# Kernel tuning notes

Measured on AMD Instinct MI355X. Metric: run time of the kernel, lower is better.

Reference implementation:

```python
import jax, jax.numpy as jnp
import numpy as np
import math

EMB = 64
NEG_INF = -1e30

def _layernorm(x, g, b, eps=1e-5):
    mu = jnp.mean(x, axis=-1, keepdims=True)
    var = jnp.mean((x - mu) ** 2, axis=-1, keepdims=True)
    return (x - mu) * jax.lax.rsqrt(var + eps) * g + b

def setup_inputs() -> dict:
    key = jax.random.key(0)
    ks = jax.random.split(key, 8)
    b, t, n, d = 16, 12, 307, EMB
    s = 1.0 / math.sqrt(d)
    inp = {
        'x': jax.random.normal(ks[0], (b, t, n, d), dtype=jnp.float32),
        'stg': jax.random.uniform(ks[1], (b, n, t, n), dtype=jnp.float32),
        'topk': 3,
        'q_w': jax.random.normal(ks[2], (d, d), dtype=jnp.float32) * s,
        'q_b': jnp.zeros((d,), jnp.float32),
        'k_w': jax.random.normal(ks[3], (d, d), dtype=jnp.float32) * s,
        'k_b': jnp.zeros((d,), jnp.float32),
        'ln_g': jnp.ones((d,), jnp.float32),
        'ln_b': jnp.zeros((d,), jnp.float32),
        'ffn_ln_g': jnp.ones((d,), jnp.float32),
        'ffn_ln_b': jnp.zeros((d,), jnp.float32),
        'fc1_w': jax.random.normal(ks[4], (4 * d, d), dtype=jnp.float32) * s,
        'fc1_b': jnp.zeros((4 * d,), jnp.float32),
        'fc2_w': jax.random.normal(ks[5], (d, 4 * d), dtype=jnp.float32) * (0.5 * s),
        'fc2_b': jnp.zeros((d,), jnp.float32),
    }
    return inp

def reference(x, stg, topk, q_w, q_b, k_w, k_b, ln_g, ln_b, ffn_ln_g, ffn_ln_b, fc1_w, fc1_b, fc2_w, fc2_b):
    b, t, n, d = x.shape
    scale = 1.0 / math.sqrt(d)
    x_ = _layernorm(x, ln_g, ln_b)           # [b,t,n,d]
    y_ = x_[:, -1]                            # [b,n,d] last timestep
    q = y_ @ q_w.T + q_b                      # [b,n,d]
    k = x_ @ k_w.T + k_b                      # [b,t,n,d]
    dg = jnp.einsum('bnd,btmd->bntm', q, k) * scale
    sag = jax.nn.sigmoid(dg) * stg * scale    # gated scores [b,n,t,n]
    sag = sag.reshape(b, n, t * n)
    if topk > 0:
        kk = topk * n if topk < 5 else topk   # mirrors torch's self.topk *= n
        top_values, _ = jax.lax.top_k(sag, kk)
        thr = top_values[..., -1:]
        sag = jnp.where(sag > thr, sag, NEG_INF)  # strict >, as in torch code
    sag = jax.nn.softmax(sag, axis=-1).reshape(b, n, t, n)  # dropout in eval mode = identity
    o = jnp.einsum('bntm,btmd->bnd', sag, x_)
    h = o + y_
    # FFN: pre-norm residual MLP (LayerNorm -> Linear(d,4d) -> ReLU -> Linear(4d,d) + residual)
    z = _layernorm(h, ffn_ln_g, ffn_ln_b)
    z = jax.nn.relu(z @ fc1_w.T + fc1_b) @ fc2_w.T + fc2_b
    return h + z
```

## Files before the change

### kernel.cpp

```cpp
#include <hip/hip_runtime.h>

typedef __bf16 bf16x8 __attribute__((ext_vector_type(8)));
typedef float  f32x4  __attribute__((ext_vector_type(4)));
typedef unsigned short u16x8 __attribute__((ext_vector_type(8)));

constexpr int BB    = 16;
constexpr int TT    = 12;
constexpr int NN    = 307;
constexpr int TN    = TT * NN;
constexpr int ROWSX = BB * TT * NN;
constexpr int ROWSH = BB * NN;
constexpr int SST1  = 3712;
constexpr int SSTR  = 3840;
constexpr int HPS   = ROWSH * 64;
constexpr int KQ    = 928;
constexpr float SCALE = 0.125f;

__device__ __forceinline__ float wred_sum(float v) {
#pragma unroll
    for (int m = 32; m > 0; m >>= 1) v += __shfl_xor(v, m, 64);
    return v;
}

__global__ void fold_k(const float* __restrict__ qw, const float* __restrict__ qb,
                       const float* __restrict__ kw, const float* __restrict__ kb,
                       float* __restrict__ M, float* __restrict__ b2,
                       float* __restrict__ vv, float* __restrict__ cc) {
    int e = blockIdx.x, d = threadIdx.x;
    float acc = 0.f;
    for (int dp = 0; dp < 64; ++dp) acc += qw[dp * 64 + e] * kw[dp * 64 + d];
    M[e * 64 + d] = acc;
    float vp = wred_sum(qw[d * 64 + e] * kb[d]);
    if (d == 0) vv[e] = vp;
    if (e == 0) {
        float b = 0.f;
        for (int dp = 0; dp < 64; ++dp) b += qb[dp] * kw[dp * 64 + d];
        b2[d] = b;
        float cp = wred_sum(qb[d] * kb[d]);
        if (d == 0) *cc = cp;
    }
}

__global__ void wconv_k(const float* __restrict__ fc1w, const float* __restrict__ fc2w,
                        __bf16* __restrict__ fc1b16, __bf16* __restrict__ fc2b16) {
    int i = blockIdx.x * 256 + threadIdx.x;
    if (i < 16384) fc1b16[i] = (__bf16)fc1w[i];
    else fc2b16[i - 16384] = (__bf16)fc2w[i - 16384];
}

__global__ __launch_bounds__(256) void ln_k(const float* __restrict__ x,
                                            const float* __restrict__ g,
                                            const float* __restrict__ b,
                                            __bf16* __restrict__ xnb,
                                            float* __restrict__ y32) {
    int w = threadIdx.x >> 6, l = threadIdx.x & 63;
    int r = blockIdx.x * 4 + w;
    if (r >= ROWSX) return;
    float val = x[r * 64 + l];
    float mu  = wred_sum(val) * (1.f / 64.f);
    float dv  = val - mu;
    float var = wred_sum(dv * dv) * (1.f / 64.f);
    float xv  = dv * rsqrtf(var + 1e-5f) * g[l] + b[l];
    xnb[(size_t)r * 64 + l] = (__bf16)xv;
    int t = (r / NN) % TT;
    if (t == TT - 1) {
        int bbv = r / (NN * TT), n = r % NN;
        y32[(bbv * NN + n) * 64 + l] = xv;
    }
}

__global__ __launch_bounds__(256) void t_k(const __bf16* __restrict__ xnb,
                                           __bf16* __restrict__ xnT) {
    __shared__ unsigned short tile[64][65];
    int bb = blockIdx.y, j0 = blockIdx.x * 64, t = threadIdx.x;
    const unsigned short* src = (const unsigned short*)xnb;
    unsigned short* dst = (unsigned short*)xnT;
#pragma unroll
    for (int i = 0; i < 16; ++i) {
        int f = t + 256 * i, jr = f >> 6, dc = f & 63;
        int j = j0 + jr;
        tile[jr][dc] = (j < TN) ? src[((size_t)bb * TN + j) * 64 + dc] : (unsigned short)0;
    }
    __syncthreads();
#pragma unroll
    for (int i = 0; i < 16; ++i) {
        int f = t + 256 * i, d = f >> 6, jj = f & 63;
        dst[((size_t)bb * 64 + d) * SSTR + j0 + jj] = tile[jj][d];
    }
}

__global__ __launch_bounds__(256) void qt_k(const float* __restrict__ y32,
                                            const float* __restrict__ M,
                                            const float* __restrict__ b2,
                                            const float* __restrict__ vv,
                                            const float* __restrict__ ccp,
                                            __bf16* __restrict__ qtb,
                                            float* __restrict__ cq) {
    int w = threadIdx.x >> 6, l = threadIdx.x & 63;
    int rr = blockIdx.x * 4 + w;
    if (rr >= ROWSH) return;
    float y = y32[rr * 64 + l];
    float acc = b2[l];
#pragma unroll
    for (int e = 0; e < 64; ++e) acc += __shfl(y, e, 64) * M[e * 64 + l];
    qtb[(size_t)rr * 64 + l] = (__bf16)acc;
    float cp = wred_sum(y * vv[l]);
    if (l == 0) cq[rr] = cp + *ccp;
}

__global__ __launch_bounds__(256) void score_k(const __bf16* __restrict__ qtb,
                                               const float* __restrict__ cq,
                                               const __bf16* __restrict__ xnb,
                                               const float* __restrict__ stg,
                                               __bf16* __restrict__ sag) {
    __shared__ unsigned short wb[64 * 136];
    int bb = blockIdx.z, n0 = blockIdx.y * 64, j0 = blockIdx.x * 128;
    int t = threadIdx.x;
    int w = t >> 6, lane = t & 63;
    int m16 = lane & 15, q4 = lane >> 4;

    const bf16x8* ap = (const bf16x8*)(qtb + ((size_t)bb * NN + n0 + w * 16 + m16) * 64);
    bf16x8 a0 = ap[q4], a1 = ap[q4 + 4];
    f32x4 acc[8];
#pragma unroll
    for (int jt = 0; jt < 8; ++jt) {
        const bf16x8* bp = (const bf16x8*)(xnb + ((size_t)bb * TN + j0 + jt * 16 + m16) * 64);
        bf16x8 b0 = bp[q4], b1 = bp[q4 + 4];
        f32x4 c = {0.f, 0.f, 0.f, 0.f};
        c = __builtin_amdgcn_mfma_f32_16x16x32_bf16(a0, b0, c, 0, 0, 0);
        c = __builtin_amdgcn_mfma_f32_16x16x32_bf16(a1, b1, c, 0, 0, 0);
        acc[jt] = c;
    }
    int nbase = n0 + w * 16 + q4 * 4;
    float cn[4];
#pragma unroll
    for (int r = 0; r < 4; ++r) {
        int n = nbase + r;
        cn[r] = (n < NN) ? cq[bb * NN + n] : 0.f;
    }

    const float* stgb = stg + (size_t)bb * NN * TN;
#pragma unroll
    for (int r = 0; r < 4; ++r) {
        int nloc = w * 16 + q4 * 4 + r;
        const float* srow = stgb + (size_t)min(nbase + r, NN - 1) * TN;
        u16x8 wvr;
#pragma unroll
        for (int jt = 0; jt < 8; ++jt) {
            int j = j0 + jt * 16 + m16;
            float sv = (j < TN) ? srow[j] : 0.f;
            float dg = (acc[jt][r] + cn[r]) * SCALE;
            float s  = 1.f / (1.f + __expf(-dg));
            float wv = (j < TN) ? s * sv * SCALE : 0.f;
            __bf16 wb16 = (__bf16)wv;
            wvr[jt] = *(unsigned short*)&wb16;
        }
#pragma unroll
        for (int jt = 0; jt < 8; ++jt)
            wb[nloc * 136 + jt * 16 + m16] = wvr[jt];
    }
    __syncthreads();

#pragma unroll
    for (int i = 0; i < 4; ++i) {
        int chunk = t + i * 256;
        int row = chunk >> 4, c8 = (chunk & 15) * 8;
        int n = n0 + row;
        if (n < NN) {
            u16x8 v = *(const u16x8*)&wb[row * 136 + c8];
            *(u16x8*)((unsigned short*)sag + (size_t)(bb * NN + n) * SST1 + j0 + c8) = v;
        }
    }
}

__global__ __launch_bounds__(256) void smax_k(__bf16* __restrict__ sagB,
                                              const int* __restrict__ topk_p,
                                              float* __restrict__ rsum) {
    int t = threadIdx.x;
    int wid = t >> 6, lane = t & 63;
    int row = blockIdx.x * 4 + wid;
    if (row >= ROWSH) return;

    int topkv = *topk_p;
    bool selAll = (topkv <= 0);
    int kk = 0;
    if (!selAll) {
        kk = (topkv < 5) ? topkv * NN : topkv;
        if (kk > TN) kk = TN;
    }

    u16x8* src = (u16x8*)((unsigned short*)sagB + (size_t)row * SST1);
    u16x8 va[8];
#pragma unroll
    for (int ci = 0; ci < 8; ++ci) {
        int c = lane + (ci << 6);
        u16x8 v = {0, 0, 0, 0, 0, 0, 0, 0};
        if (c < 464) v = src[c];
        va[ci] = v;
    }
    int vmb = 0;
#pragma unroll
    for (int ci = 0; ci < 8; ++ci)
#pragma unroll
        for (int e = 0; e < 8; ++e) vmb = max(vmb, (int)va[ci][e]);
#pragma unroll
    for (int m = 32; m > 0; m >>= 1) vmb = max(vmb, __shfl_xor(vmb, m, 64));
    float vmax = __uint_as_float(((unsigned)vmb) << 16);

    unsigned thrb = 0;
    if (!selAll) {
        unsigned lo = 0, hi = (unsigned)vmb;
        while (lo < hi) {
            unsigned mid = (lo + hi) >> 1;
            int cnt = 0;
#pragma unroll
            for (int ci = 0; ci < 8; ++ci)
#pragma unroll
                for (int e = 0; e < 8; ++e)
                    cnt += (int)__popcll(__ballot((unsigned)va[ci][e] > mid));
            if (cnt < kk) hi = mid; else lo = mid + 1;
        }
        thrb = lo;
    }

    float local = 0.f;
#pragma unroll
    for (int ci = 0; ci < 8; ++ci) {
        int c = lane + (ci << 6);
        int nvv = (c < 460) ? 8 : ((c == 460) ? 4 : 0);
#pragma unroll
        for (int e = 0; e < 8; ++e) {
            unsigned u = va[ci][e];
            bool sel = selAll ? (e < nvv) : (u > thrb);
            float ev = sel ? __expf(__uint_as_float(u << 16) - vmax) : 0.f;
            local += ev;
            __bf16 eb = (__bf16)ev;
            va[ci][e] = *(unsigned short*)&eb;
        }
    }
    local = wred_sum(local);
    bool uni = !(local > 0.f);
    if (lane == 0) rsum[row] = uni ? (float)TN : local;

    if (uni) {
        __bf16 one = (__bf16)1.f, zero = (__bf16)0.f;
#pragma unroll
        for (int ci = 0; ci < 8; ++ci) {
            int c = lane + (ci << 6);
            if (c < 464) {
                int nvv = (c < 460) ? 8 : ((c == 460) ? 4 : 0);
                bf16x8 o;
#pragma unroll
                for (int e = 0; e < 8; ++e) o[e] = (e < nvv) ? one : zero;
                *(bf16x8*)&src[c] = o;
            }
        }
    } else {
#pragma unroll
        for (int ci = 0; ci < 8; ++ci) {
            int c = lane + (ci << 6);
            if (c < 464) src[c] = va[ci];
        }
    }
}

__global__ __launch_bounds__(256) void pv_k(const __bf16* __restrict__ sagB,
                                            const __bf16* __restrict__ xnT,
                                            const float* __restrict__ y32,
                                            const float* __restrict__ rsum,
                                            float* __restrict__ hp) {
    int bb = blockIdx.z, kq = blockIdx.y, n0 = blockIdx.x * 16;
    int wid = threadIdx.x >> 6, lane = threadIdx.x & 63;
    int m16 = lane & 15, q4 = lane >> 4;

    int arow = min(n0 + m16, NN - 1);
    const __bf16* ab  = sagB + (size_t)(bb * NN + arow) * SST1 + kq * KQ + q4 * 8;
    const __bf16* bbp = xnT + ((size_t)bb * 64 + wid * 16 + m16) * SSTR + kq * KQ + q4 * 8;

    f32x4 acc0 = {0.f, 0.f, 0.f, 0.f}, acc1 = {0.f, 0.f, 0.f, 0.f};
#pragma unroll 4
    for (int ks = 0; ks < 29; ++ks) {
        bf16x8 a = *(const bf16x8*)(ab + ks * 32);
        bf16x8 b = *(const bf16x8*)(bbp + ks * 32);
        if (ks & 1) acc1 = __builtin_amdgcn_mfma_f32_16x16x32_bf16(a, b, acc1, 0, 0, 0);
        else        acc0 = __builtin_amdgcn_mfma_f32_16x16x32_bf16(a, b, acc0, 0, 0, 0);
    }
#pragma unroll
    for (int r = 0; r < 4; ++r) {
        int n = n0 + q4 * 4 + r;
        if (n < NN) {
            size_t o = (size_t)(bb * NN + n) * 64 + wid * 16 + m16;
            float inv = 1.f / rsum[bb * NN + n];
            float v = (acc0[r] + acc1[r]) * inv;
            if (kq == 0) v += y32[o];
            hp[(size_t)kq * HPS + o] = v;
        }
    }
}

__global__ __launch_bounds__(256) void ffn_k(const float* __restrict__ hp,
                                             const float* __restrict__ g,
                                             const float* __restrict__ bln,
                                             const __bf16* __restrict__ fc1b16,
                                             const float* __restrict__ fc1b,
                                             const __bf16* __restrict__ fc2b16,
                                             const float* __restrict__ fc2b,
                                             float* __restrict__ out) {
    __shared__ __bf16 zb[16 * 68];
    __shared__ __bf16 ab[16 * 264];
    int t = threadIdx.x, r0 = blockIdx.x * 16;
    int wid = t >> 6, lane = t & 63;
    int m16 = lane & 15, q4 = lane >> 4;

#pragma unroll
    for (int q = 0; q < 4; ++q) {
        int rl = wid * 4 + q;
        size_t i = (size_t)(r0 + rl) * 64 + lane;
        float val = hp[i] + hp[HPS + i] + hp[2 * HPS + i] + hp[3 * HPS + i];
        float mu  = wred_sum(val) * (1.f / 64.f);
        float dv  = val - mu;
        float var = wred_sum(dv * dv) * (1.f / 64.f);
        zb[rl * 68 + lane] = (__bf16)(dv * rsqrtf(var + 1e-5f) * g[lane] + bln[lane]);
    }
    __syncthreads();

    bf16x8 a0 = *(const bf16x8*)&zb[m16 * 68 + q4 * 8];
    bf16x8 a1 = *(const bf16x8*)&zb[m16 * 68 + 32 + q4 * 8];
#pragma unroll
    for (int jt2 = 0; jt2 < 4; ++jt2) {
        int j0t = (wid * 4 + jt2) * 16;
        const __bf16* bp = fc1b16 + (size_t)(j0t + m16) * 64 + q4 * 8;
        f32x4 c = {0.f, 0.f, 0.f, 0.f};
        c = __builtin_amdgcn_mfma_f32_16x16x32_bf16(a0, *(const bf16x8*)bp, c, 0, 0, 0);
        c = __builtin_amdgcn_mfma_f32_16x16x32_bf16(a1, *(const bf16x8*)(bp + 32), c, 0, 0, 0);
        int j = j0t + m16;
        float bias = fc1b[j];
#pragma unroll
        for (int r = 0; r < 4; ++r)
            ab[(q4 * 4 + r) * 264 + j] = (__bf16)fmaxf(c[r] + bias, 0.f);
    }
    __syncthreads();

    f32x4 c2a = {0.f, 0.f, 0.f, 0.f}, c2b = {0.f, 0.f, 0.f, 0.f};
    const __bf16* b2p = fc2b16 + (size_t)(wid * 16 + m16) * 256 + q4 * 8;
#pragma unroll
    for (int k8 = 0; k8 < 8; k8 += 2) {
        bf16x8 aa0 = *(const bf16x8*)&ab[m16 * 264 + k8 * 32 + q4 * 8];
        bf16x8 aa1 = *(const bf16x8*)&ab[m16 * 264 + (k8 + 1) * 32 + q4 * 8];
        c2a = __builtin_amdgcn_mfma_f32_16x16x32_bf16(aa0, *(const bf16x8*)(b2p + k8 * 32), c2a, 0, 0, 0);
        c2b = __builtin_amdgcn_mfma_f32_16x16x32_bf16(aa1, *(const bf16x8*)(b2p + (k8 + 1) * 32), c2b, 0, 0, 0);
    }
    int d = wid * 16 + m16;
    float bias2 = fc2b[d];
#pragma unroll
    for (int r = 0; r < 4; ++r) {
        size_t row = (size_t)(r0 + q4 * 4 + r);
        size_t o = row * 64 + d;
        float hsum = hp[o] + hp[HPS + o] + hp[2 * HPS + o] + hp[3 * HPS + o];
        out[o] = hsum + c2a[r] + c2b[r] + bias2;
    }
}

extern "C" void kernel_launch(void* const* d_in, const int* in_sizes, int n_in,
                              void* d_out, int out_size, void* d_ws, size_t ws_size,
                              hipStream_t stream) {
    const float* x    = (const float*)d_in[0];
    const float* stg  = (const float*)d_in[1];
    const int*   topk = (const int*)d_in[2];
    const float* qw   = (const float*)d_in[3];
    const float* qb   = (const float*)d_in[4];
    const float* kw   = (const float*)d_in[5];
    const float* kb   = (const float*)d_in[6];
    const float* lng  = (const float*)d_in[7];
    const float* lnb  = (const float*)d_in[8];
    const float* flng = (const float*)d_in[9];
    const float* flnb = (const float*)d_in[10];
    const float* fc1w = (const float*)d_in[11];
    const float* fc1b = (const float*)d_in[12];
    const float* fc2w = (const float*)d_in[13];
    const float* fc2b = (const float*)d_in[14];
    float* out = (float*)d_out;

    float* ws = (float*)d_ws;
    __bf16* xnb = (__bf16*)ws;
    float* p1   = ws + 1886208;
    __bf16* xnT = (__bf16*)p1;
    float* p2   = p1 + 1966080;
    __bf16* qtb = (__bf16*)p2;
    float* y32  = p2 + 157696;
    float* cq   = y32 + 314368;
    float* M    = cq + 4928;
    float* b2   = M + 4096;
    float* vv   = b2 + 64;
    float* cc   = vv + 64;
    __bf16* fc1b16 = (__bf16*)(cc + 16);
    __bf16* fc2b16 = (__bf16*)((float*)fc1b16 + 8192);
    __bf16* sag = (__bf16*)((float*)fc2b16 + 8192);
    float* hp   = (float*)sag + 9116672;
    float* rsum = hp + 4 * HPS;

    fold_k<<<64, 64, 0, stream>>>(qw, qb, kw, kb, M, b2, vv, cc);
    wconv_k<<<128, 256, 0, stream>>>(fc1w, fc2w, fc1b16, fc2b16);
    ln_k<<<(ROWSX + 3) / 4, 256, 0, stream>>>(x, lng, lnb, xnb, y32);
    t_k<<<dim3((TN + 63) / 64, BB), 256, 0, stream>>>(xnb, xnT);
    qt_k<<<(ROWSH + 3) / 4, 256, 0, stream>>>(y32, M, b2, vv, cc, qtb, cq);
    score_k<<<dim3((TN + 127) / 128, (NN + 63) / 64, BB), 256, 0, stream>>>(qtb, cq, xnb, stg, sag);
    smax_k<<<(ROWSH + 3) / 4, 256, 0, stream>>>(sag, topk, rsum);
    pv_k<<<dim3((NN + 15) / 16, 4, BB), 256, 0, stream>>>(sag, xnT, y32, rsum, hp);
    ffn_k<<<ROWSH / 16, 256, 0, stream>>>(hp, flng, flnb, fc1b16, fc1b, fc2b16, fc2b, out);
}
```

Before: 269.0 us.

## Fuse layernorm with transpose and swap MFMA operands for coalesced stg loads

Merges the layernorm kernel and the transpose kernel into one, so normalized rows go straight into the shared-memory tile and the transpose no longer has to re-read xnb from global memory. It also swaps the MFMA operand roles in score_k so that each lane's output elements lie along j. That lets stg be read with float4 loads and the bf16 results be written to LDS as 4-wide stores, with the row padding changed to 144. The cost is a smaller LN grid that does serial wave reductions per row.

Result: no change. 266.4 us (-1.0%).

```diff
diff --git a/kernel.cpp b/kernel.cpp
--- a/kernel.cpp
+++ b/kernel.cpp
@@ -3,6 +3,7 @@
 typedef __bf16 bf16x8 __attribute__((ext_vector_type(8)));
 typedef float  f32x4  __attribute__((ext_vector_type(4)));
 typedef unsigned short u16x8 __attribute__((ext_vector_type(8)));
+typedef unsigned short u16x4 __attribute__((ext_vector_type(4)));
 
 constexpr int BB    = 16;
 constexpr int TT    = 12;
@@ -48,38 +49,35 @@
     else fc2b16[i - 16384] = (__bf16)fc2w[i - 16384];
 }
 
-__global__ __launch_bounds__(256) void ln_k(const float* __restrict__ x,
-                                            const float* __restrict__ g,
-                                            const float* __restrict__ b,
-                                            __bf16* __restrict__ xnb,
-                                            float* __restrict__ y32) {
-    int w = threadIdx.x >> 6, l = threadIdx.x & 63;
-    int r = blockIdx.x * 4 + w;
-    if (r >= ROWSX) return;
-    float val = x[r * 64 + l];
-    float mu  = wred_sum(val) * (1.f / 64.f);
-    float dv  = val - mu;
-    float var = wred_sum(dv * dv) * (1.f / 64.f);
-    float xv  = dv * rsqrtf(var + 1e-5f) * g[l] + b[l];
-    xnb[(size_t)r * 64 + l] = (__bf16)xv;
-    int t = (r / NN) % TT;
-    if (t == TT - 1) {
-        int bbv = r / (NN * TT), n = r % NN;
-        y32[(bbv * NN + n) * 64 + l] = xv;
-    }
-}
-
-__global__ __launch_bounds__(256) void t_k(const __bf16* __restrict__ xnb,
-                                           __bf16* __restrict__ xnT) {
+__global__ __launch_bounds__(256) void lnt_k(const float* __restrict__ x,
+                                             const float* __restrict__ g,
+                                             const float* __restrict__ b,
+                                             __bf16* __restrict__ xnb,
+                                             __bf16* __restrict__ xnT,
+                                             float* __restrict__ y32) {
     __shared__ unsigned short tile[64][65];
     int bb = blockIdx.y, j0 = blockIdx.x * 64, t = threadIdx.x;
-    const unsigned short* src = (const unsigned short*)xnb;
+    int w = t >> 6, lane = t & 63;
+    float gg = g[lane], bbv = b[lane];
     unsigned short* dst = (unsigned short*)xnT;
-#pragma unroll
+#pragma unroll 4
     for (int i = 0; i < 16; ++i) {
-        int f = t + 256 * i, jr = f >> 6, dc = f & 63;
+        int jr = w * 16 + i;
         int j = j0 + jr;
-        tile[jr][dc] = (j < TN) ? src[((size_t)bb * TN + j) * 64 + dc] : (unsigned short)0;
+        bool valid = (j < TN);
+        float val = valid ? x[((size_t)bb * TN + j) * 64 + lane] : 0.f;
+        float mu  = wred_sum(val) * (1.f / 64.f);
+        float dv  = val - mu;
+        float var = wred_sum(dv * dv) * (1.f / 64.f);
+        float xv  = dv * rsqrtf(var + 1e-5f) * gg + bbv;
+        if (valid) {
+            __bf16 xb = (__bf16)xv;
+            xnb[((size_t)bb * TN + j) * 64 + lane] = xb;
+            tile[jr][lane] = *(unsigned short*)&xb;
+            if (j >= 11 * NN) y32[((size_t)bb * NN + (j - 11 * NN)) * 64 + lane] = xv;
+        } else {
+            tile[jr][lane] = 0;
+        }
     }
     __syncthreads();
 #pragma unroll
@@ -113,51 +111,57 @@
                                                const __bf16* __restrict__ xnb,
                                                const float* __restrict__ stg,
                                                __bf16* __restrict__ sag) {
-    __shared__ unsigned short wb[64 * 136];
+    __shared__ unsigned short wb[64 * 144];
     int bb = blockIdx.z, n0 = blockIdx.y * 64, j0 = blockIdx.x * 128;
     int t = threadIdx.x;
     int w = t >> 6, lane = t & 63;
     int m16 = lane & 15, q4 = lane >> 4;
 
-    const bf16x8* ap = (const bf16x8*)(qtb + ((size_t)bb * NN + n0 + w * 16 + m16) * 64);
-    bf16x8 a0 = ap[q4], a1 = ap[q4 + 4];
-    f32x4 acc[8];
-#pragma unroll
-    for (int jt = 0; jt < 8; ++jt) {
-        const bf16x8* bp = (const bf16x8*)(xnb + ((size_t)bb * TN + j0 + jt * 16 + m16) * 64);
+    bf16x8 a[2][2];
+#pragma unroll
+    for (int jj = 0; jj < 2; ++jj) {
+        const bf16x8* ap = (const bf16x8*)(xnb + ((size_t)bb * TN + j0 + (w * 2 + jj) * 16 + m16) * 64);
+        a[jj][0] = ap[q4];
+        a[jj][1] = ap[q4 + 4];
+    }
+
+    f32x4 acc[2][4];
+#pragma unroll
+    for (int nt = 0; nt < 4; ++nt) {
+        const bf16x8* bp = (const bf16x8*)(qtb + ((size_t)bb * NN + n0 + nt * 16 + m16) * 64);
         bf16x8 b0 = bp[q4], b1 = bp[q4 + 4];
-        f32x4 c = {0.f, 0.f, 0.f, 0.f};
-        c = __builtin_amdgcn_mfma_f32_16x16x32_bf16(a0, b0, c, 0, 0, 0);
-        c = __builtin_amdgcn_mfma_f32_16x16x32_bf16(a1, b1, c, 0, 0, 0);
-        acc[jt] = c;
-    }
-    int nbase = n0 + w * 16 + q4 * 4;
-    float cn[4];
-#pragma unroll
-    for (int r = 0; r < 4; ++r) {
-        int n = nbase + r;
-        cn[r] = (n < NN) ? cq[bb * NN + n] : 0.f;
+#pragma unroll
+        for (int jj = 0; jj < 2; ++jj) {
+            f32x4 c = {0.f, 0.f, 0.f, 0.f};
+            c = __builtin_amdgcn_mfma_f32_16x16x32_bf16(a[jj][0], b0, c, 0, 0, 0);
+            c = __builtin_amdgcn_mfma_f32_16x16x32_bf16(a[jj][1], b1, c, 0, 0, 0);
+            acc[jj][nt] = c;
+        }
     }
 
     const float* stgb = stg + (size_t)bb * NN * TN;
 #pragma unroll
-    for (int r = 0; r < 4; ++r) {
-        int nloc = w * 16 + q4 * 4 + r;
-        const float* srow = stgb + (size_t)min(nbase + r, NN - 1) * TN;
-        u16x8 wvr;
-#pragma unroll
-        for (int jt = 0; jt < 8; ++jt) {
-            int j = j0 + jt * 16 + m16;
-            float sv = (j < TN) ? srow[j] : 0.f;
-            float dg = (acc[jt][r] + cn[r]) * SCALE;
-            float s  = 1.f / (1.f + __expf(-dg));
-            float wv = (j < TN) ? s * sv * SCALE : 0.f;
-            __bf16 wb16 = (__bf16)wv;
-            wvr[jt] = *(unsigned short*)&wb16;
-        }
-#pragma unroll
-        for (int jt = 0; jt < 8; ++jt)
-            wb[nloc * 136 + jt * 16 + m16] = wvr[jt];
+    for (int nt = 0; nt < 4; ++nt) {
+        int n = n0 + nt * 16 + m16;
+        float cnv = (n < NN) ? cq[bb * NN + n] : 0.f;
+        const float* srow = stgb + (size_t)min(n, NN - 1) * TN;
+#pragma unroll
+        for (int jj = 0; jj < 2; ++jj) {
+            int jb = j0 + (w * 2 + jj) * 16 + q4 * 4;
+            float4 sv = {0.f, 0.f, 0.f, 0.f};
+            if (jb < TN) sv = *(const float4*)(srow + jb);
+            u16x4 hw;
+            float svv[4] = {sv.x, sv.y, sv.z, sv.w};
+#pragma unroll
+            for (int r = 0; r < 4; ++r) {
+                float dg = (acc[jj][nt][r] + cnv) * SCALE;
+                float s  = 1.f / (1.f + __expf(-dg));
+                float wv = (jb + r < TN) ? s * svv[r] * SCALE : 0.f;
+                __bf16 wb16 = (__bf16)wv;
+                hw[r] = *(unsigned short*)&wb16;
+            }
+            *(u16x4*)&wb[(nt * 16 + m16) * 144 + (w * 2 + jj) * 16 + q4 * 4] = hw;
+        }
     }
     __syncthreads();
 
@@ -167,7 +171,7 @@
         int row = chunk >> 4, c8 = (chunk & 15) * 8;
         int n = n0 + row;
         if (n < NN) {
-            u16x8 v = *(const u16x8*)&wb[row * 136 + c8];
+            u16x8 v = *(const u16x8*)&wb[row * 144 + c8];
             *(u16x8*)((unsigned short*)sag + (size_t)(bb * NN + n) * SST1 + j0 + c8) = v;
         }
     }
@@ -401,8 +405,7 @@
 
     fold_k<<<64, 64, 0, stream>>>(qw, qb, kw, kb, M, b2, vv, cc);
     wconv_k<<<128, 256, 0, stream>>>(fc1w, fc2w, fc1b16, fc2b16);
-    ln_k<<<(ROWSX + 3) / 4, 256, 0, stream>>>(x, lng, lnb, xnb, y32);
-    t_k<<<dim3((TN + 63) / 64, BB), 256, 0, stream>>>(xnb, xnT);
+    lnt_k<<<dim3(58, BB), 256, 0, stream>>>(x, lng, lnb, xnb, xnT, y32);
     qt_k<<<(ROWSH + 3) / 4, 256, 0, stream>>>(y32, M, b2, vv, cc, qtb, cq);
     score_k<<<dim3((TN + 127) / 128, (NN + 63) / 64, BB), 256, 0, stream>>>(qtb, cq, xnb, stg, sag);
     smax_k<<<(ROWSH + 3) / 4, 256, 0, stream>>>(sag, topk, rsum);
```
